# Performance work log

Measured on AMD Instinct MI355X. Metric: run time of the kernel, lower is better.

## Reference

```python
import jax, jax.numpy as jnp
import numpy as np
import math

B, W, N = 48, 100, 1000
EMB, H, QKV, LOCAL = 128, 8, 16, 100
L = LOCAL + 1  # depot + local_size neighbors


def pos_enc(length):
    # sinusoidal positional encoding, emb_dim even so no pad needed
    nts = EMB // 2
    inv = jnp.exp(jnp.arange(nts, dtype=jnp.float32) * (-math.log(10000.0) / max(nts - 1, 1)))
    pos = jnp.arange(length, dtype=jnp.float32)
    st = pos[:, None] * inv[None, :]
    return jnp.concatenate([jnp.sin(st), jnp.cos(st)], axis=1)  # [length, EMB]


def setup_inputs() -> dict:
    key = jax.random.key(0)
    ks = jax.random.split(key, 11)
    return {
        "theta": jax.random.uniform(ks[0], (B, W, N), dtype=jnp.float32),
        "dist": jax.random.uniform(ks[1], (B, W, N), dtype=jnp.float32),
        "xy": jax.random.uniform(ks[2], (B, W, N, 2), dtype=jnp.float32),
        "norm_demand": jax.random.uniform(ks[3], (B, W, N), dtype=jnp.float32),
        "ninf_mask": jnp.zeros((B, W, N), jnp.float32),
        "init_w": jax.random.normal(ks[4], (3, EMB), dtype=jnp.float32) * 0.1,
        "init_b": jnp.zeros((EMB,), jnp.float32),
        "cur_token": jax.random.uniform(ks[5], (EMB,), minval=-1.0, maxval=1.0, dtype=jnp.float32),
        "Wq": jax.random.normal(ks[6], (EMB, H * QKV), dtype=jnp.float32) * 0.05,
        "Wk": jax.random.normal(ks[7], (EMB, H * QKV), dtype=jnp.float32) * 0.05,
        "Wv": jax.random.normal(ks[8], (EMB, H * QKV), dtype=jnp.float32) * 0.05,
        "Wc_w": jax.random.normal(ks[9], (H * QKV, EMB), dtype=jnp.float32) * 0.05,
        "Wc_b": jnp.zeros((EMB,), jnp.float32),
    }


def reference(theta, dist, xy, norm_demand, ninf_mask, init_w, init_b, cur_token, Wq, Wk, Wv, Wc_w, Wc_b):
    # depot always masked: dist -= mask => depot distance -> +inf
    mask = ninf_mask.at[:, :, 0].set(-jnp.inf)
    dist_eff = dist - mask  # [B,W,N]

    # k smallest distances among non-depot nodes (topk largest=False)
    neg_vals, idx0 = jax.lax.top_k(-dist_eff[:, :, 1:], LOCAL)
    dvals = -neg_vals
    dvals = jnp.where(jnp.isinf(dvals), 0.0, dvals)
    norm_on = (jnp.max(dvals, axis=-1) != 0.0)[..., None]          # [B,W,1]
    norm_fac = jnp.max(dvals, axis=-1, keepdims=True) + 1e-6       # [B,W,1]

    depot = jnp.zeros((B, W, 1), idx0.dtype)
    idx = jnp.concatenate([depot, idx0 + 1], axis=-1)              # [B,W,L]

    g = lambda a: jnp.take_along_axis(a, idx, axis=-1)
    sd = g(dist_eff)
    sdem = g(norm_demand)
    sm = g(ninf_mask)
    sx = g(xy[..., 0])
    sy = g(xy[..., 1])

    # zero out inf entries (the masked depot slot)
    infm = jnp.isinf(sd)
    sdem = jnp.where(infm, 0.0, sdem)
    sx = jnp.where(infm, 0.0, sx)
    sy = jnp.where(infm, 0.0, sy)

    # per-(b,w) coordinate normalization by max local distance
    sx = jnp.where(norm_on, sx / norm_fac, sx)
    sy = jnp.where(norm_on, sy / norm_fac, sy)

    # euclidean + demand => 3 input features
    sorted_input = jnp.stack([sx, sy, sdem], axis=-1)              # [B,W,L,3]
    init_k = sorted_input @ init_w + init_b + pos_enc(L)[None, None]  # [B,W,L,EMB]

    # cur_token is identical for every (b,w) -> shared query per head
    q = (cur_token @ Wq).reshape(H, QKV)
    k = (init_k @ Wk).reshape(B, W, L, H, QKV)
    v = (init_k @ Wv).reshape(B, W, L, H, QKV)

    score = jnp.einsum('hd,bwlhd->bwhl', q, k) / float(np.sqrt(QKV)) + sm[:, :, None, :]
    attn = jax.nn.softmax(score, axis=-1)
    out = jnp.einsum('bwhl,bwlhd->bwhd', attn, v).reshape(B, W, H * QKV)

    mh = out @ Wc_w + Wc_b                                         # [B,W,EMB]
    score2 = jnp.einsum('bwe,bwle->bwl', mh, init_k) / float(np.sqrt(EMB))

    bi = jnp.arange(B)[:, None, None]
    wi = jnp.arange(W)[None, :, None]
    return jnp.zeros((B, W, N), score2.dtype).at[bi, wi, idx].set(score2)
```

## Files before the change

### kernel.cpp

```cpp
#include <hip/hip_runtime.h>
#include <math.h>

#define Bb   48
#define Ww   100
#define Nn   1000
#define EMB  128
#define Hh   8
#define LL   101
#define LOCALK 100
#define TPB  256

typedef _Float16 half2v __attribute__((ext_vector_type(2)));
typedef _Float16 half8v __attribute__((ext_vector_type(8)));

#define WS_A    0
#define WS_PE   1024
#define WS_AC   13952
#define WS_WVI  13984
#define WS_PV   14496
#define WS_PEA  27808
#define WS_WG   28616
#define WS_BG   31688
#define WS_PEH  31816
#define WS_PEG2 38280

__device__ __forceinline__ unsigned f2key(float x) {
    unsigned u = __float_as_uint(x);
    return (u & 0x80000000u) ? ~u : (u | 0x80000000u);
}
__device__ __forceinline__ float key2f(unsigned k) {
    unsigned u = (k & 0x80000000u) ? (k & 0x7fffffffu) : ~k;
    return __uint_as_float(u);
}

__global__ void setup1(const float* __restrict__ cur, const float* __restrict__ Wq,
                       const float* __restrict__ Wk, const float* __restrict__ iw,
                       const float* __restrict__ ib, const float* __restrict__ Wv,
                       float* __restrict__ ws) {
    const int t = threadIdx.x, b = blockIdx.x;
    if (b == 0) {
        __shared__ float qs[EMB];
        __shared__ float as_[Hh * EMB];
        if (t < EMB) {
            float acc = 0.f;
            for (int e = 0; e < EMB; ++e) acc += cur[e] * Wq[e * EMB + t];
            qs[t] = acc;
        }
        __syncthreads();
        for (int i = t; i < Hh * EMB; i += TPB) {
            int h = i >> 7, e = i & 127;
            float acc = 0.f;
            for (int d = 0; d < 16; ++d) acc += Wk[e * EMB + h * 16 + d] * qs[h * 16 + d];
            acc *= 0.25f;
            as_[i] = acc; ws[WS_A + i] = acc;
        }
        __syncthreads();
        if (t < 32) {
            int i = t >> 3, h = t & 7;
            const float* src = (i == 0) ? iw : (i == 1) ? iw + EMB : (i == 2) ? iw + 2 * EMB : ib;
            float acc = 0.f;
            for (int e = 0; e < EMB; ++e) acc += src[e] * as_[h * EMB + e];
            ws[WS_AC + t] = acc;
        }
    } else {
        int base = (b - 1) * TPB + t;
        const float kneg = -0.14619587891040738f;
        if (base < LL * EMB) {
            int l = base >> 7, c = base & 127, ic = c & 63;
            float inv = expf((float)ic * kneg);
            float v = (float)l * inv;
            float r = (c < 64) ? sinf(v) : cosf(v);
            ws[WS_PE + base] = r;
            ((_Float16*)(ws + WS_PEH))[base] = (_Float16)r;
        } else if (base < LL * EMB + 512) {
            int j = base - LL * EMB;
            int iv = j >> 7, hd = j & 127;
            const float* src = (iv == 0) ? iw : (iv == 1) ? iw + EMB : (iv == 2) ? iw + 2 * EMB : ib;
            float acc = 0.f;
            for (int e = 0; e < EMB; ++e) acc += src[e] * Wv[e * EMB + hd];
            ws[WS_WVI + j] = acc;
        }
    }
}

__global__ void setup2a(const float* __restrict__ Wv, float* __restrict__ ws) {
    int idx = blockIdx.x * TPB + threadIdx.x;
    if (idx < 128 * LL) {
        int l = idx >> 7, hd = idx & 127;
        const float* pr = ws + WS_PE + l * EMB;
        float acc = 0.f;
        for (int e = 0; e < EMB; ++e) acc += pr[e] * Wv[e * EMB + hd];
        ws[WS_PV + hd * 104 + l] = acc;
    } else if (idx < 128 * LL + Hh * LL) {
        int j = idx - 128 * LL;
        int h = j / LL, l = j - h * LL;
        const float* pr = ws + WS_PE + l * EMB;
        const float* ar = ws + WS_A + h * EMB;
        float acc = 0.f;
        for (int e = 0; e < EMB; ++e) acc += pr[e] * ar[e];
        ws[WS_PEA + j] = acc;
    }
}

__global__ void setup2b(const float* __restrict__ Wcw, const float* __restrict__ Wcb,
                        float* __restrict__ ws) {
    int idx = blockIdx.x * TPB + threadIdx.x;
    if (idx < 816 * 128) {
        int hl = idx >> 7, e = idx & 127;
        float acc = 0.f;
        if (hl < 808) {
            int h = hl / LL, l = hl - h * LL;
            for (int d = 0; d < 16; ++d)
                acc += ws[WS_PV + (h * 16 + d) * 104 + l] * Wcw[(h * 16 + d) * EMB + e];
        }
        ((_Float16*)(ws + WS_PEG2))[(hl >> 3) * 1024 + e * 8 + (hl & 7)] = (_Float16)acc;
    } else if (idx < 816 * 128 + 3072) {
        int j = idx - 816 * 128;
        int iwg = j >> 10, r = j & 1023, h = r >> 7, e = r & 127;
        float acc = 0.f;
        for (int d = 0; d < 16; ++d)
            acc += ws[WS_WVI + iwg * 128 + h * 16 + d] * Wcw[(h * 16 + d) * EMB + e];
        ws[WS_WG + j] = acc;
    } else if (idx < 816 * 128 + 3072 + 128) {
        int e = idx - (816 * 128 + 3072);
        float acc = Wcb[e];
        for (int hd = 0; hd < 128; ++hd) acc += ws[WS_WVI + 384 + hd] * Wcw[hd * EMB + e];
        ws[WS_BG + e] = acc;
    }
}

__global__ __launch_bounds__(TPB, 8) void main_kernel(
    const float* __restrict__ dist,
    const float* __restrict__ xy,
    const float* __restrict__ ndem,
    const float* __restrict__ ninf,
    const float* __restrict__ iw,
    const float* __restrict__ ib,
    const float* __restrict__ ws,
    float* __restrict__ out) {

    const int bw   = blockIdx.x;
    const int tid  = threadIdx.x;
    const int lane = tid & 63;
    const int wid  = tid >> 6;
    const float* distRow = dist + (size_t)bw * Nn;
    const float* maskRow = ninf + (size_t)bw * Nn;
    float*       outRow  = out  + (size_t)bw * Nn;

    __shared__ int   hist4[4 * 256];
    __shared__ unsigned long long list[104];
    __shared__ int   sel[LL];
    __shared__ float feat3[3 * LL];
    __shared__ float smk[LL];
    __shared__ __align__(16) _Float16 attnh[816];
    __shared__ float mhf[EMB];
    __shared__ __align__(16) _Float16 mhh[EMB];
    __shared__ float partial[2][EMB];
    __shared__ float cAC[32];
    __shared__ float coef[Hh][3];
    __shared__ float coefM[4];
    __shared__ int   selSh[3];
    __shared__ int   waveSums[4];
    __shared__ float red[2];
    __shared__ unsigned long long pivotSh;
    __shared__ int   cntSh;

    for (int i = tid; i < Nn; i += TPB) outRow[i] = 0.f;

    unsigned long long rk[4];
    #pragma unroll
    for (int r = 0; r < 4; ++r) {
        int i = tid + 256 * r;
        unsigned long long kv = ~0ull;
        if (i >= 1 && i < Nn) {
            float de = distRow[i] - maskRow[i];
            kv = ((unsigned long long)f2key(de) << 32) | (unsigned)i;
        }
        rk[r] = kv;
    }
    #pragma unroll
    for (int r = 0; r < 4; ++r) hist4[tid + 256 * r] = 0;
    __syncthreads();

    unsigned long long prefix = 0;
    int shift = 56;
    int remRank = 99;
    int* myhist = hist4 + (wid << 8);
    for (int round = 0; round < 8; ++round) {
        shift = 56 - 8 * round;
        #pragma unroll
        for (int r = 0; r < 4; ++r) {
            unsigned long long kv = rk[r];
            if (round == 0 || (kv >> (shift + 8)) == (prefix >> (shift + 8)))
                atomicAdd(&myhist[(unsigned)((kv >> shift) & 0xffull)], 1);
        }
        __syncthreads();
        int cnt = hist4[tid] + hist4[256 + tid] + hist4[512 + tid] + hist4[768 + tid];
        hist4[tid] = 0; hist4[256 + tid] = 0; hist4[512 + tid] = 0; hist4[768 + tid] = 0;
        int v = cnt;
        #pragma unroll
        for (int o = 1; o < 64; o <<= 1) {
            int t = __shfl_up(v, o, 64);
            if (lane >= o) v += t;
        }
        if (lane == 63) waveSums[wid] = v;
        __syncthreads();
        int wOff = 0;
        if (wid > 0) wOff += waveSums[0];
        if (wid > 1) wOff += waveSums[1];
        if (wid > 2) wOff += waveSums[2];
        int excl = v + wOff - cnt;
        if (cnt > 0 && remRank >= excl && remRank < excl + cnt) {
            selSh[0] = tid; selSh[1] = excl; selSh[2] = cnt;
        }
        __syncthreads();
        prefix |= ((unsigned long long)selSh[0]) << shift;
        remRank -= selSh[1];
        if (selSh[2] == 1) break;
    }
    #pragma unroll
    for (int r = 0; r < 4; ++r)
        if ((rk[r] >> shift) == (prefix >> shift)) pivotSh = rk[r];
    if (tid == 0) cntSh = 0;
    __syncthreads();
    const unsigned long long pivot = pivotSh;

    #pragma unroll
    for (int r = 0; r < 4; ++r) {
        bool p = rk[r] <= pivot;
        unsigned long long m = __ballot(p);
        int c = __popcll(m);
        int base = 0;
        if (lane == 0 && c) base = atomicAdd(&cntSh, c);
        base = __shfl(base, 0, 64);
        if (p) list[base + __popcll(m & ((1ull << lane) - 1ull))] = rk[r];
    }
    __syncthreads();

    if (tid < 128) {
        float dvm = 0.f;
        if (tid < LOCALK) {
            unsigned long long kv = list[tid];
            int rank = 0;
            for (int j = 0; j < LOCALK; ++j) rank += (list[j] < kv) ? 1 : 0;
            float v = key2f((unsigned)(kv >> 32));
            bool infm = isinf(v);
            sel[rank + 1] = (int)(unsigned)(kv & 0xffffffffu) | (infm ? 0x40000000 : 0);
            dvm = infm ? 0.f : v;
        }
        #pragma unroll
        for (int o = 32; o > 0; o >>= 1) dvm = fmaxf(dvm, __shfl_xor(dvm, o, 64));
        if (lane == 0) red[wid] = dvm;
    }
    if (tid == 0) sel[0] = 0x40000000;
    __syncthreads();

    const float nmax = fmaxf(red[0], red[1]);
    const bool  norm_on = (nmax != 0.f);
    const float nfac = nmax + 1e-6f;

    if (tid < LL) {
        int s = sel[tid];
        int n = s & 0xffffff;
        bool infm = (s & 0x40000000) != 0;
        float fx = 0.f, fy = 0.f, fd = 0.f;
        if (!infm) {
            size_t base = (size_t)bw * Nn + n;
            fx = xy[2 * base];
            fy = xy[2 * base + 1];
            fd = ndem[base];
        }
        if (norm_on) { fx /= nfac; fy /= nfac; }
        feat3[tid] = fx; feat3[LL + tid] = fy; feat3[2 * LL + tid] = fd;
        smk[tid] = maskRow[n];
    }
    if (tid >= 224) cAC[tid - 224] = ws[WS_AC + tid - 224];
    __syncthreads();

    {
        int g = tid >> 5, ln = tid & 31;
        int l0 = ln, l1 = ln + 32, l2 = ln + 64, l3 = ln + 96;
        bool ok3 = (l3 < LL);
        const float* pea = ws + WS_PEA + g * LL;
        float A0 = cAC[g], A1 = cAC[8 + g], A2 = cAC[16 + g], C = cAC[24 + g];
        float v0 = feat3[l0] * A0 + feat3[LL + l0] * A1 + feat3[2 * LL + l0] * A2 + C + pea[l0] + smk[l0];
        float v1 = feat3[l1] * A0 + feat3[LL + l1] * A1 + feat3[2 * LL + l1] * A2 + C + pea[l1] + smk[l1];
        float v2 = feat3[l2] * A0 + feat3[LL + l2] * A1 + feat3[2 * LL + l2] * A2 + C + pea[l2] + smk[l2];
        float v3 = ok3 ? (feat3[l3] * A0 + feat3[LL + l3] * A1 + feat3[2 * LL + l3] * A2 + C + pea[l3] + smk[l3])
                       : -INFINITY;
        float m = fmaxf(fmaxf(v0, v1), fmaxf(v2, v3));
        #pragma unroll
        for (int o = 16; o > 0; o >>= 1) m = fmaxf(m, __shfl_xor(m, o, 32));
        float e0 = __expf(v0 - m), e1 = __expf(v1 - m), e2 = __expf(v2 - m);
        float e3 = ok3 ? __expf(v3 - m) : 0.f;
        float s = e0 + e1 + e2 + e3;
        #pragma unroll
        for (int o = 16; o > 0; o >>= 1) s += __shfl_xor(s, o, 32);
        float inv = 1.f / s;
        e0 *= inv; e1 *= inv; e2 *= inv; e3 *= inv;
        attnh[g * LL + l0] = (_Float16)e0;
        attnh[g * LL + l1] = (_Float16)e1;
        attnh[g * LL + l2] = (_Float16)e2;
        if (ok3) attnh[g * LL + l3] = (_Float16)e3;
        if (tid < 8) attnh[808 + tid] = (_Float16)0.f;
        #pragma unroll
        for (int f = 0; f < 3; ++f) {
            const float* fr = feat3 + f * LL;
            float cs = e0 * fr[l0] + e1 * fr[l1] + e2 * fr[l2] + (ok3 ? e3 * fr[l3] : 0.f);
            #pragma unroll
            for (int o = 16; o > 0; o >>= 1) cs += __shfl_xor(cs, o, 32);
            if (ln == 0) coef[g][f] = cs;
        }
    }
    __syncthreads();

    {
        int sd = tid >> 7, e = tid & 127;
        const half8v* pbase = (const half8v*)(ws + WS_PEG2) + (size_t)(sd * 51) * 128 + e;
        const half8v* aav = (const half8v*)attnh + sd * 51;
        float c0 = 0.f, c1 = 0.f, c2 = 0.f, c3 = 0.f;
        #pragma unroll 2
        for (int j = 0; j < 51; ++j) {
            half8v p = pbase[(size_t)j * 128];
            half8v a = aav[j];
            c0 = __builtin_amdgcn_fdot2(__builtin_shufflevector(p, p, 0, 1),
                                        __builtin_shufflevector(a, a, 0, 1), c0, false);
            c1 = __builtin_amdgcn_fdot2(__builtin_shufflevector(p, p, 2, 3),
                                        __builtin_shufflevector(a, a, 2, 3), c1, false);
            c2 = __builtin_amdgcn_fdot2(__builtin_shufflevector(p, p, 4, 5),
                                        __builtin_shufflevector(a, a, 4, 5), c2, false);
            c3 = __builtin_amdgcn_fdot2(__builtin_shufflevector(p, p, 6, 7),
                                        __builtin_shufflevector(a, a, 6, 7), c3, false);
        }
        partial[sd][e] = (c0 + c1) + (c2 + c3);
    }
    __syncthreads();

    if (tid < EMB) {
        float m = ws[WS_BG + tid] + partial[0][tid] + partial[1][tid];
        #pragma unroll
        for (int h = 0; h < Hh; ++h) {
            m += coef[h][0] * ws[WS_WG + (0 * 8 + h) * EMB + tid]
               + coef[h][1] * ws[WS_WG + (1 * 8 + h) * EMB + tid]
               + coef[h][2] * ws[WS_WG + (2 * 8 + h) * EMB + tid];
        }
        mhf[tid] = m; mhh[tid] = (_Float16)m;
    }
    __syncthreads();

    {
        int g = tid >> 6;
        const float* src = (g == 0) ? iw : (g == 1) ? iw + EMB : (g == 2) ? iw + 2 * EMB : ib;
        float v = mhf[lane] * src[lane] + mhf[lane + 64] * src[lane + 64];
        #pragma unroll
        for (int o = 32; o > 0; o >>= 1) v += __shfl_xor(v, o, 64);
        if (lane == 0) coefM[g] = v;
    }
    __syncthreads();

    if (tid < LL) {
        float base = feat3[tid] * coefM[0] + feat3[LL + tid] * coefM[1]
                   + feat3[2 * LL + tid] * coefM[2] + coefM[3];
        const half2v* pr = (const half2v*)(ws + WS_PEH) + tid * 64;
        const half2v* mr = (const half2v*)mhh;
        float c0 = 0.f, c1 = 0.f, c2 = 0.f, c3 = 0.f;
        #pragma unroll
        for (int j = 0; j < 64; j += 4) {
            c0 = __builtin_amdgcn_fdot2(pr[j],     mr[j],     c0, false);
            c1 = __builtin_amdgcn_fdot2(pr[j + 1], mr[j + 1], c1, false);
            c2 = __builtin_amdgcn_fdot2(pr[j + 2], mr[j + 2], c2, false);
            c3 = __builtin_amdgcn_fdot2(pr[j + 3], mr[j + 3], c3, false);
        }
        outRow[sel[tid] & 0xffffff] = (base + (c0 + c1) + (c2 + c3)) * 0.08838834764831845f;
    }
}

extern "C" void kernel_launch(void* const* d_in, const int* in_sizes, int n_in,
                              void* d_out, int out_size, void* d_ws, size_t ws_size,
                              hipStream_t stream) {
    const float* dist  = (const float*)d_in[1];
    const float* xy    = (const float*)d_in[2];
    const float* ndem  = (const float*)d_in[3];
    const float* ninf  = (const float*)d_in[4];
    const float* initw = (const float*)d_in[5];
    const float* initb = (const float*)d_in[6];
    const float* cur   = (const float*)d_in[7];
    const float* Wq    = (const float*)d_in[8];
    const float* Wk    = (const float*)d_in[9];
    const float* Wv    = (const float*)d_in[10];
    const float* Wcw   = (const float*)d_in[11];
    const float* Wcb   = (const float*)d_in[12];
    float* out = (float*)d_out;
    float* ws  = (float*)d_ws;

    hipLaunchKernelGGL(setup1,  dim3(56),  dim3(TPB), 0, stream, cur, Wq, Wk, initw, initb, Wv, ws);
    hipLaunchKernelGGL(setup2a, dim3(54),  dim3(TPB), 0, stream, Wv, ws);
    hipLaunchKernelGGL(setup2b, dim3(421), dim3(TPB), 0, stream, Wcw, Wcb, ws);
    hipLaunchKernelGGL(main_kernel, dim3(Bb * Ww), dim3(TPB), 0, stream,
                       dist, xy, ndem, ninf, initw, initb, ws, out);
}
```

Measured before the change: 110.0 us.

## Refactor attention output path into per-head PV then Wc matvec, stage output row in LDS

Drops the precomputed PE·Wv·Wc table (816x128 fp16) and the per-block read of it. Each block now computes the attention-weighted value vector per head from a smaller fp16 PE·Wv table, then applies the Wc projection as a 128x128 fp16 matvec. The output row is built in shared memory, reusing the histogram buffer, and written once with coalesced float4 stores, replacing the scattered writes after a separate zeroing pass. It also shrinks the setup kernels, at the cost of an extra sync and dependent matvec stage inside the main kernel.

```diff
diff --git a/kernel.cpp b/kernel.cpp
--- a/kernel.cpp
+++ b/kernel.cpp
@@ -17,12 +17,10 @@
 #define WS_PE   1024
 #define WS_AC   13952
 #define WS_WVI  13984
-#define WS_PV   14496
-#define WS_PEA  27808
-#define WS_WG   28616
-#define WS_BG   31688
-#define WS_PEH  31816
-#define WS_PEG2 38280
+#define WS_PEA  14496
+#define WS_PEH  15304
+#define WS_PVH  21768
+#define WS_WCT  28424
 
 __device__ __forceinline__ unsigned f2key(float x) {
     unsigned u = __float_as_uint(x);
@@ -31,6 +29,17 @@
 __device__ __forceinline__ float key2f(unsigned k) {
     unsigned u = (k & 0x80000000u) ? (k & 0x7fffffffu) : ~k;
     return __uint_as_float(u);
+}
+__device__ __forceinline__ void dot8(float& c0, float& c1, float& c2, float& c3,
+                                     half8v p, half8v a) {
+    c0 = __builtin_amdgcn_fdot2(__builtin_shufflevector(p, p, 0, 1),
+                                __builtin_shufflevector(a, a, 0, 1), c0, false);
+    c1 = __builtin_amdgcn_fdot2(__builtin_shufflevector(p, p, 2, 3),
+                                __builtin_shufflevector(a, a, 2, 3), c1, false);
+    c2 = __builtin_amdgcn_fdot2(__builtin_shufflevector(p, p, 4, 5),
+                                __builtin_shufflevector(a, a, 4, 5), c2, false);
+    c3 = __builtin_amdgcn_fdot2(__builtin_shufflevector(p, p, 6, 7),
+                                __builtin_shufflevector(a, a, 6, 7), c3, false);
 }
 
 __global__ void setup1(const float* __restrict__ cur, const float* __restrict__ Wq,
@@ -85,14 +94,16 @@
 
 __global__ void setup2a(const float* __restrict__ Wv, float* __restrict__ ws) {
     int idx = blockIdx.x * TPB + threadIdx.x;
-    if (idx < 128 * LL) {
-        int l = idx >> 7, hd = idx & 127;
-        const float* pr = ws + WS_PE + l * EMB;
+    if (idx < 128 * 104) {
+        int hd = idx / 104, l = idx - hd * 104;
         float acc = 0.f;
-        for (int e = 0; e < EMB; ++e) acc += pr[e] * Wv[e * EMB + hd];
-        ws[WS_PV + hd * 104 + l] = acc;
-    } else if (idx < 128 * LL + Hh * LL) {
-        int j = idx - 128 * LL;
+        if (l < LL) {
+            const float* pr = ws + WS_PE + l * EMB;
+            for (int e = 0; e < EMB; ++e) acc += pr[e] * Wv[e * EMB + hd];
+        }
+        ((_Float16*)(ws + WS_PVH))[idx] = (_Float16)acc;
+    } else if (idx < 128 * 104 + Hh * LL) {
+        int j = idx - 128 * 104;
         int h = j / LL, l = j - h * LL;
         const float* pr = ws + WS_PE + l * EMB;
         const float* ar = ws + WS_A + h * EMB;
@@ -102,30 +113,11 @@
     }
 }
 
-__global__ void setup2b(const float* __restrict__ Wcw, const float* __restrict__ Wcb,
-                        float* __restrict__ ws) {
+__global__ void setup2b(const float* __restrict__ Wcw, float* __restrict__ ws) {
     int idx = blockIdx.x * TPB + threadIdx.x;
-    if (idx < 816 * 128) {
-        int hl = idx >> 7, e = idx & 127;
-        float acc = 0.f;
-        if (hl < 808) {
-            int h = hl / LL, l = hl - h * LL;
-            for (int d = 0; d < 16; ++d)
-                acc += ws[WS_PV + (h * 16 + d) * 104 + l] * Wcw[(h * 16 + d) * EMB + e];
-        }
-        ((_Float16*)(ws + WS_PEG2))[(hl >> 3) * 1024 + e * 8 + (hl & 7)] = (_Float16)acc;
-    } else if (idx < 816 * 128 + 3072) {
-        int j = idx - 816 * 128;
-        int iwg = j >> 10, r = j & 1023, h = r >> 7, e = r & 127;
-        float acc = 0.f;
-        for (int d = 0; d < 16; ++d)
-            acc += ws[WS_WVI + iwg * 128 + h * 16 + d] * Wcw[(h * 16 + d) * EMB + e];
-        ws[WS_WG + j] = acc;
-    } else if (idx < 816 * 128 + 3072 + 128) {
-        int e = idx - (816 * 128 + 3072);
-        float acc = Wcb[e];
-        for (int hd = 0; hd < 128; ++hd) acc += ws[WS_WVI + 384 + hd] * Wcw[hd * EMB + e];
-        ws[WS_BG + e] = acc;
+    if (idx < 128 * 128) {
+        int e = idx >> 7, hd = idx & 127;
+        ((_Float16*)(ws + WS_WCT))[idx] = (_Float16)Wcw[hd * EMB + e];
     }
 }
 
@@ -136,6 +128,7 @@
     const float* __restrict__ ninf,
     const float* __restrict__ iw,
     const float* __restrict__ ib,
+    const float* __restrict__ Wcb,
     const float* __restrict__ ws,
     float* __restrict__ out) {
 
@@ -147,15 +140,18 @@
     const float* maskRow = ninf + (size_t)bw * Nn;
     float*       outRow  = out  + (size_t)bw * Nn;
 
-    __shared__ int   hist4[4 * 256];
+    __shared__ __align__(16) char u0[4096];
+    int*   hist4 = (int*)u0;
+    float* row   = (float*)u0;
+
     __shared__ unsigned long long list[104];
     __shared__ int   sel[LL];
     __shared__ float feat3[3 * LL];
     __shared__ float smk[LL];
-    __shared__ __align__(16) _Float16 attnh[816];
+    __shared__ __align__(16) _Float16 attnh[Hh * 104];
+    __shared__ __align__(16) _Float16 uhh[EMB];
     __shared__ float mhf[EMB];
     __shared__ __align__(16) _Float16 mhh[EMB];
-    __shared__ float partial[2][EMB];
     __shared__ float cAC[32];
     __shared__ float coef[Hh][3];
     __shared__ float coefM[4];
@@ -164,8 +160,6 @@
     __shared__ float red[2];
     __shared__ unsigned long long pivotSh;
     __shared__ int   cntSh;
-
-    for (int i = tid; i < Nn; i += TPB) outRow[i] = 0.f;
 
     unsigned long long rk[4];
     #pragma unroll
@@ -251,6 +245,10 @@
         #pragma unroll
         for (int o = 32; o > 0; o >>= 1) dvm = fmaxf(dvm, __shfl_xor(dvm, o, 64));
         if (lane == 0) red[wid] = dvm;
+    } else {
+        float4 z = make_float4(0.f, 0.f, 0.f, 0.f);
+        float4* r4 = (float4*)row;
+        for (int i = tid - 128; i < 250; i += 128) r4[i] = z;
     }
     if (tid == 0) sel[0] = 0x40000000;
     __syncthreads();
@@ -298,11 +296,11 @@
         for (int o = 16; o > 0; o >>= 1) s += __shfl_xor(s, o, 32);
         float inv = 1.f / s;
         e0 *= inv; e1 *= inv; e2 *= inv; e3 *= inv;
-        attnh[g * LL + l0] = (_Float16)e0;
-        attnh[g * LL + l1] = (_Float16)e1;
-        attnh[g * LL + l2] = (_Float16)e2;
-        if (ok3) attnh[g * LL + l3] = (_Float16)e3;
-        if (tid < 8) attnh[808 + tid] = (_Float16)0.f;
+        attnh[g * 104 + l0] = (_Float16)e0;
+        attnh[g * 104 + l1] = (_Float16)e1;
+        attnh[g * 104 + l2] = (_Float16)e2;
+        if (ok3) attnh[g * 104 + l3] = (_Float16)e3;
+        else if (l3 < 104) attnh[g * 104 + l3] = (_Float16)0.f;
         #pragma unroll
         for (int f = 0; f < 3; ++f) {
             const float* fr = feat3 + f * LL;
@@ -314,37 +312,31 @@
     }
     __syncthreads();
 
-    {
-        int sd = tid >> 7, e = tid & 127;
-        const half8v* pbase = (const half8v*)(ws + WS_PEG2) + (size_t)(sd * 51) * 128 + e;
-        const half8v* aav = (const half8v*)attnh + sd * 51;
+    if (tid < 128) {
+        int hd = tid, h = hd >> 4;
+        const half8v* pv = (const half8v*)((const _Float16*)(ws + WS_PVH) + hd * 104);
+        const half8v* at = (const half8v*)(attnh + h * 104);
         float c0 = 0.f, c1 = 0.f, c2 = 0.f, c3 = 0.f;
-        #pragma unroll 2
-        for (int j = 0; j < 51; ++j) {
-            half8v p = pbase[(size_t)j * 128];
-            half8v a = aav[j];
-            c0 = __builtin_amdgcn_fdot2(__builtin_shufflevector(p, p, 0, 1),
-                                        __builtin_shufflevector(a, a, 0, 1), c0, false);
-            c1 = __builtin_amdgcn_fdot2(__builtin_shufflevector(p, p, 2, 3),
-                                        __builtin_shufflevector(a, a, 2, 3), c1, false);
-            c2 = __builtin_amdgcn_fdot2(__builtin_shufflevector(p, p, 4, 5),
-                                        __builtin_shufflevector(a, a, 4, 5), c2, false);
-            c3 = __builtin_amdgcn_fdot2(__builtin_shufflevector(p, p, 6, 7),
-                                        __builtin_shufflevector(a, a, 6, 7), c3, false);
-        }
-        partial[sd][e] = (c0 + c1) + (c2 + c3);
-    }
-    __syncthreads();
-
-    if (tid < EMB) {
-        float m = ws[WS_BG + tid] + partial[0][tid] + partial[1][tid];
-        #pragma unroll
-        for (int h = 0; h < Hh; ++h) {
-            m += coef[h][0] * ws[WS_WG + (0 * 8 + h) * EMB + tid]
-               + coef[h][1] * ws[WS_WG + (1 * 8 + h) * EMB + tid]
-               + coef[h][2] * ws[WS_WG + (2 * 8 + h) * EMB + tid];
-        }
-        mhf[tid] = m; mhh[tid] = (_Float16)m;
+        #pragma unroll
+        for (int j = 0; j < 13; ++j) dot8(c0, c1, c2, c3, pv[j], at[j]);
+        float u = (c0 + c1) + (c2 + c3)
+                + coef[h][0] * ws[WS_WVI + hd]
+                + coef[h][1] * ws[WS_WVI + 128 + hd]
+                + coef[h][2] * ws[WS_WVI + 256 + hd]
+                + ws[WS_WVI + 384 + hd];
+        uhh[hd] = (_Float16)u;
+    }
+    __syncthreads();
+
+    if (tid < 128) {
+        int e = tid;
+        const half8v* wr = (const half8v*)((const _Float16*)(ws + WS_WCT) + e * 128);
+        const half8v* ur = (const half8v*)uhh;
+        float c0 = 0.f, c1 = 0.f, c2 = 0.f, c3 = 0.f;
+        #pragma unroll
+        for (int j = 0; j < 16; ++j) dot8(c0, c1, c2, c3, wr[j], ur[j]);
+        float m = Wcb[e] + (c0 + c1) + (c2 + c3);
+        mhf[e] = m; mhh[e] = (_Float16)m;
     }
     __syncthreads();
 
@@ -361,17 +353,17 @@
     if (tid < LL) {
         float base = feat3[tid] * coefM[0] + feat3[LL + tid] * coefM[1]
                    + feat3[2 * LL + tid] * coefM[2] + coefM[3];
-        const half2v* pr = (const half2v*)(ws + WS_PEH) + tid * 64;
-        const half2v* mr = (const half2v*)mhh;
+        const half8v* pr = (const half8v*)((const _Float16*)(ws + WS_PEH) + tid * 128);
+        const half8v* mr = (const half8v*)mhh;
         float c0 = 0.f, c1 = 0.f, c2 = 0.f, c3 = 0.f;
         #pragma unroll
-        for (int j = 0; j < 64; j += 4) {
-            c0 = __builtin_amdgcn_fdot2(pr[j],     mr[j],     c0, false);
-            c1 = __builtin_amdgcn_fdot2(pr[j + 1], mr[j + 1], c1, false);
-            c2 = __builtin_amdgcn_fdot2(pr[j + 2], mr[j + 2], c2, false);
-            c3 = __builtin_amdgcn_fdot2(pr[j + 3], mr[j + 3], c3, false);
-        }
-        outRow[sel[tid] & 0xffffff] = (base + (c0 + c1) + (c2 + c3)) * 0.08838834764831845f;
+        for (int j = 0; j < 16; ++j) dot8(c0, c1, c2, c3, pr[j], mr[j]);
+        row[sel[tid] & 0xffffff] = (base + (c0 + c1) + (c2 + c3)) * 0.08838834764831845f;
+    }
+    __syncthreads();
+
+    if (tid < 250) {
+        ((float4*)outRow)[tid] = ((float4*)row)[tid];
     }
 }
 
@@ -393,9 +385,9 @@
     float* out = (float*)d_out;
     float* ws  = (float*)d_ws;
 
-    hipLaunchKernelGGL(setup1,  dim3(56),  dim3(TPB), 0, stream, cur, Wq, Wk, initw, initb, Wv, ws);
-    hipLaunchKernelGGL(setup2a, dim3(54),  dim3(TPB), 0, stream, Wv, ws);
-    hipLaunchKernelGGL(setup2b, dim3(421), dim3(TPB), 0, stream, Wcw, Wcb, ws);
+    hipLaunchKernelGGL(setup1,  dim3(56), dim3(TPB), 0, stream, cur, Wq, Wk, initw, initb, Wv, ws);
+    hipLaunchKernelGGL(setup2a, dim3(56), dim3(TPB), 0, stream, Wv, ws);
+    hipLaunchKernelGGL(setup2b, dim3(64), dim3(TPB), 0, stream, Wcw, ws);
     hipLaunchKernelGGL(main_kernel, dim3(Bb * Ww), dim3(TPB), 0, stream,
-                       dist, xy, ndem, ninf, initw, initb, ws, out);
-}
+                       dist, xy, ndem, ninf, initw, initb, Wcb, ws, out);
+}
```

Result: faster. 104.4 us (-5.1%).
